# Kernel optimization log

Measured on AMD Instinct MI355X. Metric: run time of the kernel, lower is better.

Reference implementation:

```python
import jax, jax.numpy as jnp
import numpy as np

B, S, R, Z, NLHS = 1024, 277, 76, 56, 24  # batch, seq_len, n_rules, z_size, n_lhs_symbols


def setup_inputs() -> dict:
    key = jax.random.key(0)
    k1, k2, k3, k4, k5, k6 = jax.random.split(key, 6)
    model_out_x = jax.random.normal(k1, (B, S, R), jnp.float32)
    mu = jax.random.normal(k2, (B, Z), jnp.float32)
    log_var = 0.1 * jax.random.normal(k3, (B, Z), jnp.float32)
    # one-hot targets over rules
    tgt_idx = jax.random.randint(k4, (B, S), 0, R)
    target_x = jax.nn.one_hot(tgt_idx, R, dtype=jnp.float32)
    # binary allowed-transition masks per LHS symbol
    masks = (jax.random.uniform(k5, (NLHS, R)) < 0.3).astype(jnp.float32)
    masks = masks.at[:, 0].set(1.0)  # ensure no all-zero mask row
    ind_to_lhs_ind = jax.random.randint(k6, (R,), 0, NLHS)
    return dict(model_out_x=model_out_x, mu=mu, log_var=log_var,
                target_x=target_x, masks=masks, ind_to_lhs_ind=ind_to_lhs_ind)


def reference(model_out_x, mu, log_var, target_x, masks, ind_to_lhs_ind):
    b = model_out_x.shape[0]
    seq_len = model_out_x.shape[1]
    z_size = mu.shape[1]

    # --- apply_masks: vectorized gather replacing the nested python loops ---
    true_rule = jnp.argmax(target_x, axis=-1)          # [B,S]
    lhs = ind_to_lhs_ind[true_rule]                    # [B,S]
    mask = masks[lhs]                                  # [B,S,R]
    shift_to_tiny = -100.0 + (model_out_x.min() - model_out_x.max())
    x = model_out_x + (1.0 - mask) * shift_to_tiny

    # --- softmax + BCE (torch BCELoss clamps log terms at -100) ---
    p = jax.nn.softmax(x, axis=-1)
    log_p = jnp.maximum(jnp.log(p), -100.0)
    log_1mp = jnp.maximum(jnp.log1p(-p), -100.0)
    bce = -jnp.mean(target_x * log_p + (1.0 - target_x) * log_1mp)
    BCE = seq_len * bce

    # --- moment-matching error on mu ---
    avg_mu = jnp.sum(mu, axis=0) / b                   # [Z]
    var = (mu.T @ mu) / b                              # [Z,Z]
    var_err = var - jnp.eye(z_size, dtype=mu.dtype)
    var_err = jnp.tanh(var_err) * var_err
    mom_err = jnp.sum(avg_mu * avg_mu) / z_size + jnp.sum(var_err) / (z_size * z_size)

    # sample_z=False, module in training mode -> loss = BCE + mom_err
    return BCE + mom_err
```

## Files before the change

kernel.cpp:

```cpp
#include <hip/hip_runtime.h>
#include <math.h>

#define BB    1024
#define SS    277
#define RR    76
#define ZZ    56
#define NLHS  24
#define NROWS (BB*SS)
#define ROWS_PER_BLOCK 64
#define NBCE (NROWS/ROWS_PER_BLOCK)
#define NMOM ZZ
#define NBLK (NBCE + NMOM)
#define V4_PER_BLOCK (ROWS_PER_BLOCK*RR/4)
#define BLK_ELEMS (ROWS_PER_BLOCK*RR)
#define TOTAL_ELEMS 21558272.0

static_assert(NROWS % ROWS_PER_BLOCK == 0, "rows divide blocks");

#define LN2F  0.69314718056f
#define NLN2F (-144.26950409f)

__global__ __launch_bounds__(256) void fused_kernel(
    const float* __restrict__ model,
    const float* __restrict__ target,
    const float* __restrict__ masks,
    const int*   __restrict__ ind_to_lhs,
    const float* __restrict__ mu,
    double* __restrict__ partials)
{
    __shared__ float         sm_x[BLK_ELEMS];
    __shared__ unsigned int  smb[NLHS*4];
    __shared__ int           sm_lhs[RR];
    __shared__ unsigned char sm_idx[ROWS_PER_BLOCK];
    __shared__ float         sm_red[4];
    __shared__ float         sdot[4][64];
    __shared__ float         ssum[4];

    const int tid = threadIdx.x;

    if (blockIdx.x >= NBCE) {
        const int j    = blockIdx.x - NBCE;
        const int w    = tid >> 6;
        const int lane = tid & 63;
        const int i    = (lane < ZZ) ? lane : 0;
        float dot = 0.f, s1 = 0.f;
        const int b0 = 256*w;
        #pragma unroll 4
        for (int b = b0; b < b0 + 256; ++b) {
            const float c = mu[b*ZZ + j];
            const float a = mu[b*ZZ + i];
            dot = fmaf(a, c, dot);
            s1 += c;
        }
        sdot[w][lane] = dot;
        if (lane == 0) ssum[w] = s1;
        __syncthreads();
        if (w == 0) {
            float term = 0.f;
            if (lane < ZZ) {
                const float var = (sdot[0][lane]+sdot[1][lane]+sdot[2][lane]+sdot[3][lane]) * (1.f/BB);
                const float ve  = var - ((lane == j) ? 1.f : 0.f);
                term = tanhf(ve) * ve * (1.f/(ZZ*ZZ));
                if (lane == j) {
                    const float am = (ssum[0]+ssum[1]+ssum[2]+ssum[3]) * (1.f/BB);
                    term = fmaf(am*am, 1.f/ZZ, term);
                }
            }
            #pragma unroll
            for (int off = 32; off; off >>= 1) term += __shfl_xor(term, off, 64);
            if (lane == 0) partials[blockIdx.x] = (double)term;
        }
        return;
    }

    if (tid < NLHS*4) smb[tid] = 0u;
    if (tid < ROWS_PER_BLOCK) sm_idx[tid] = 0;
    __syncthreads();

    for (int e = tid; e < NLHS*RR; e += 256) {
        const int lhs = e / RR;
        const int r   = e - lhs*RR;
        if (masks[e] > 0.5f)
            atomicOr(&smb[lhs*4 + (r >> 5)], 1u << (r & 31));
    }
    if (tid < RR) sm_lhs[tid] = ind_to_lhs[tid];

    const size_t blk_base = (size_t)blockIdx.x * BLK_ELEMS;

    {
        const float4* m4  = (const float4*)(model + blk_base);
        float4*       sx4 = (float4*)sm_x;
        #pragma unroll
        for (int k = 0; k < 4; ++k) sx4[tid + 256*k] = m4[tid + 256*k];
        if (tid < V4_PER_BLOCK - 1024) sx4[1024 + tid] = m4[1024 + tid];
    }

    {
        const float4* t4 = (const float4*)(target + blk_base);
        #pragma unroll
        for (int k = 0; k < 5; ++k) {
            const int v4 = tid + 256*k;
            if (v4 < V4_PER_BLOCK) {
                const float4 t = t4[v4];
                int he = -1;
                const int e = v4*4;
                if (t.x > 0.5f) he = e;
                if (t.y > 0.5f) he = e+1;
                if (t.z > 0.5f) he = e+2;
                if (t.w > 0.5f) he = e+3;
                if (he >= 0) {
                    const int row = he / RR;
                    sm_idx[row] = (unsigned char)(he - row*RR);
                }
            }
        }
    }
    __syncthreads();

    const int row    = tid >> 2;
    const int t      = tid & 3;
    const int true_r = (int)sm_idx[row];
    const int lhs    = sm_lhs[true_r];
    const unsigned int w0 = smb[lhs*4 + 0];
    const unsigned int w1 = smb[lhs*4 + 1];
    const unsigned int w2 = smb[lhs*4 + 2];

    const float4* xr = (const float4*)(sm_x + row*RR);
    float4 v[5];

    float mx = -1e30f;
    #pragma unroll
    for (int k = 0; k < 5; ++k) {
        const int c = t + 4*k;
        float4 xv = (c < 19) ? xr[c] : make_float4(-1e30f,-1e30f,-1e30f,-1e30f);
        #pragma unroll
        for (int cc = 0; cc < 4; ++cc) {
            const int r = c*4 + cc;
            const unsigned int mw = (r < 32) ? w0 : ((r < 64) ? w1 : w2);
            float* xp = (&xv.x) + cc;
            const bool un = (r < RR) && ((mw >> (r & 31)) & 1u);
            const float xm = un ? *xp : -1e30f;
            *xp = xm;
            mx = fmaxf(mx, xm);
        }
        v[k] = xv;
    }
    mx = fmaxf(mx, __shfl_xor(mx, 1, 64));
    mx = fmaxf(mx, __shfl_xor(mx, 2, 64));

    float s = 0.f;
    #pragma unroll
    for (int k = 0; k < 5; ++k) {
        #pragma unroll
        for (int cc = 0; cc < 4; ++cc) {
            float* xp = (&v[k].x) + cc;
            const float e = __expf(*xp - mx);
            *xp = e;
            s += e;
        }
    }
    s += __shfl_xor(s, 1, 64);
    s += __shfl_xor(s, 2, 64);
    const float inv = 1.f / s;

    float sum_l2 = 0.f;
    float p_true = 0.f;
    bool  owner  = false;
    #pragma unroll
    for (int k = 0; k < 5; ++k) {
        const int c = t + 4*k;
        #pragma unroll
        for (int cc = 0; cc < 4; ++cc) {
            const int r = c*4 + cc;
            const float p  = (&v[k].x)[cc] * inv;
            const float l2 = __log2f(1.f - p);
            sum_l2 += fmaxf(l2, NLN2F);
            if (r == true_r) { p_true = p; owner = true; }
        }
    }
    float row_sum = LN2F * sum_l2;
    if (owner) {
        const float l1c_t = fmaxf(LN2F * __log2f(1.f - p_true), -100.f);
        const float lp_t  = fmaxf(__logf(p_true), -100.f);
        row_sum += lp_t - l1c_t;
    }

    #pragma unroll
    for (int off = 32; off; off >>= 1) row_sum += __shfl_xor(row_sum, off, 64);
    if ((tid & 63) == 0) sm_red[tid >> 6] = row_sum;
    __syncthreads();
    if (tid == 0)
        partials[blockIdx.x] = (double)((sm_red[0] + sm_red[1]) + (sm_red[2] + sm_red[3]));
}

__global__ __launch_bounds__(256) void final_kernel(
    const double* __restrict__ partials, float* __restrict__ out)
{
    __shared__ double sred[4];
    const int tid = threadIdx.x;
    double s = 0.0;
    for (int k = tid; k < NBCE; k += 256) s += partials[k];
    double m = (tid < NMOM) ? partials[NBCE + tid] : 0.0;
    double val = s * (-(double)SS / TOTAL_ELEMS) + m;
    #pragma unroll
    for (int off = 32; off; off >>= 1) val += __shfl_xor(val, off, 64);
    if ((tid & 63) == 0) sred[tid >> 6] = val;
    __syncthreads();
    if (tid == 0) out[0] = (float)((sred[0] + sred[1]) + (sred[2] + sred[3]));
}

extern "C" void kernel_launch(void* const* d_in, const int* in_sizes, int n_in,
                              void* d_out, int out_size, void* d_ws, size_t ws_size,
                              hipStream_t stream) {
    const float* model  = (const float*)d_in[0];
    const float* mu     = (const float*)d_in[1];
    const float* target = (const float*)d_in[3];
    const float* masks  = (const float*)d_in[4];
    const int*   ind    = (const int*)  d_in[5];
    float* out  = (float*)d_out;
    double* acc = (double*)d_ws;

    fused_kernel<<<NBLK, 256, 0, stream>>>(model, target, masks, ind, mu, acc);
    final_kernel<<<1,    256, 0, stream>>>(acc, out);
}
```

Baseline: 222.6 us.

## Load rows directly to registers and process four tiles per block with prefetch

Removes the shared-memory staging of model rows and the target scan into shared memory. Each thread now loads its row slice straight from global memory into registers and finds the true rule with a per-row shuffle reduction. Each block handles four 64-row tiles and prefetches the next tile into registers while computing the current one. This amortises the per-block mask-bitmap setup and lowers shared-memory use, but the per-thread global loads are strided by row and not coalesced, and register pressure goes up.

```diff
diff --git a/kernel.cpp b/kernel.cpp
--- a/kernel.cpp
+++ b/kernel.cpp
@@ -7,15 +7,15 @@
 #define ZZ    56
 #define NLHS  24
 #define NROWS (BB*SS)
-#define ROWS_PER_BLOCK 64
-#define NBCE (NROWS/ROWS_PER_BLOCK)
+#define ROWS_PER_TILE 64
+#define TT    4
+#define TILE_ELEMS (ROWS_PER_TILE*RR)
+#define NBCE (NROWS/(ROWS_PER_TILE*TT))
 #define NMOM ZZ
 #define NBLK (NBCE + NMOM)
-#define V4_PER_BLOCK (ROWS_PER_BLOCK*RR/4)
-#define BLK_ELEMS (ROWS_PER_BLOCK*RR)
 #define TOTAL_ELEMS 21558272.0
 
-static_assert(NROWS % ROWS_PER_BLOCK == 0, "rows divide blocks");
+static_assert(NROWS % (ROWS_PER_TILE*TT) == 0, "rows divide blocks");
 
 #define LN2F  0.69314718056f
 #define NLN2F (-144.26950409f)
@@ -28,13 +28,11 @@
     const float* __restrict__ mu,
     double* __restrict__ partials)
 {
-    __shared__ float         sm_x[BLK_ELEMS];
-    __shared__ unsigned int  smb[NLHS*4];
-    __shared__ int           sm_lhs[RR];
-    __shared__ unsigned char sm_idx[ROWS_PER_BLOCK];
-    __shared__ float         sm_red[4];
-    __shared__ float         sdot[4][64];
-    __shared__ float         ssum[4];
+    __shared__ uint4 smb[NLHS];
+    __shared__ int   sm_lhs[RR];
+    __shared__ float sm_red[4];
+    __shared__ float sdot[4][64];
+    __shared__ float ssum[4];
 
     const int tid = threadIdx.x;
 
@@ -73,121 +71,130 @@
         return;
     }
 
-    if (tid < NLHS*4) smb[tid] = 0u;
-    if (tid < ROWS_PER_BLOCK) sm_idx[tid] = 0;
-    __syncthreads();
-
+    if (tid < NLHS*4) ((unsigned int*)smb)[tid] = 0u;
+    __syncthreads();
     for (int e = tid; e < NLHS*RR; e += 256) {
         const int lhs = e / RR;
         const int r   = e - lhs*RR;
         if (masks[e] > 0.5f)
-            atomicOr(&smb[lhs*4 + (r >> 5)], 1u << (r & 31));
+            atomicOr(&((unsigned int*)smb)[lhs*4 + (r >> 5)], 1u << (r & 31));
     }
     if (tid < RR) sm_lhs[tid] = ind_to_lhs[tid];
-
-    const size_t blk_base = (size_t)blockIdx.x * BLK_ELEMS;
-
+    __syncthreads();
+
+    const int rloc = tid >> 2;
+    const int t    = tid & 3;
+
+    const size_t blk_elem0 = (size_t)blockIdx.x * (TT*TILE_ELEMS) + (size_t)rloc*RR;
+
+    float acc_thread = 0.f;
+
+    float4 v[5], tv[5];
     {
-        const float4* m4  = (const float4*)(model + blk_base);
-        float4*       sx4 = (float4*)sm_x;
-        #pragma unroll
-        for (int k = 0; k < 4; ++k) sx4[tid + 256*k] = m4[tid + 256*k];
-        if (tid < V4_PER_BLOCK - 1024) sx4[1024 + tid] = m4[1024 + tid];
-    }
-
-    {
-        const float4* t4 = (const float4*)(target + blk_base);
-        #pragma unroll
-        for (int k = 0; k < 5; ++k) {
-            const int v4 = tid + 256*k;
-            if (v4 < V4_PER_BLOCK) {
-                const float4 t = t4[v4];
-                int he = -1;
-                const int e = v4*4;
-                if (t.x > 0.5f) he = e;
-                if (t.y > 0.5f) he = e+1;
-                if (t.z > 0.5f) he = e+2;
-                if (t.w > 0.5f) he = e+3;
-                if (he >= 0) {
-                    const int row = he / RR;
-                    sm_idx[row] = (unsigned char)(he - row*RR);
-                }
-            }
-        }
-    }
-    __syncthreads();
-
-    const int row    = tid >> 2;
-    const int t      = tid & 3;
-    const int true_r = (int)sm_idx[row];
-    const int lhs    = sm_lhs[true_r];
-    const unsigned int w0 = smb[lhs*4 + 0];
-    const unsigned int w1 = smb[lhs*4 + 1];
-    const unsigned int w2 = smb[lhs*4 + 2];
-
-    const float4* xr = (const float4*)(sm_x + row*RR);
-    float4 v[5];
-
-    float mx = -1e30f;
+        const float4* mr = (const float4*)(model  + blk_elem0);
+        const float4* tr = (const float4*)(target + blk_elem0);
+        #pragma unroll
+        for (int k = 0; k < 5; ++k) {
+            const int c = t + 4*k;
+            v[k]  = (c < 19) ? mr[c] : make_float4(-1e30f,-1e30f,-1e30f,-1e30f);
+            tv[k] = (c < 19) ? tr[c] : make_float4(0.f,0.f,0.f,0.f);
+        }
+    }
+
     #pragma unroll
-    for (int k = 0; k < 5; ++k) {
-        const int c = t + 4*k;
-        float4 xv = (c < 19) ? xr[c] : make_float4(-1e30f,-1e30f,-1e30f,-1e30f);
-        #pragma unroll
-        for (int cc = 0; cc < 4; ++cc) {
-            const int r = c*4 + cc;
-            const unsigned int mw = (r < 32) ? w0 : ((r < 64) ? w1 : w2);
-            float* xp = (&xv.x) + cc;
-            const bool un = (r < RR) && ((mw >> (r & 31)) & 1u);
-            const float xm = un ? *xp : -1e30f;
-            *xp = xm;
-            mx = fmaxf(mx, xm);
-        }
-        v[k] = xv;
-    }
-    mx = fmaxf(mx, __shfl_xor(mx, 1, 64));
-    mx = fmaxf(mx, __shfl_xor(mx, 2, 64));
-
-    float s = 0.f;
+    for (int tt = 0; tt < TT; ++tt) {
+        float4 vn[5], tvn[5];
+        if (tt + 1 < TT) {
+            const size_t nb = blk_elem0 + (size_t)(tt+1)*TILE_ELEMS;
+            const float4* mr = (const float4*)(model  + nb);
+            const float4* tr = (const float4*)(target + nb);
+            #pragma unroll
+            for (int k = 0; k < 5; ++k) {
+                const int c = t + 4*k;
+                vn[k]  = (c < 19) ? mr[c] : make_float4(-1e30f,-1e30f,-1e30f,-1e30f);
+                tvn[k] = (c < 19) ? tr[c] : make_float4(0.f,0.f,0.f,0.f);
+            }
+        }
+
+        int he = -1;
+        #pragma unroll
+        for (int k = 0; k < 5; ++k) {
+            const int c = t + 4*k;
+            const int e = c*4;
+            if (tv[k].x > 0.5f) he = e;
+            if (tv[k].y > 0.5f) he = e+1;
+            if (tv[k].z > 0.5f) he = e+2;
+            if (tv[k].w > 0.5f) he = e+3;
+        }
+        he = max(he, __shfl_xor(he, 1, 64));
+        he = max(he, __shfl_xor(he, 2, 64));
+        const int true_r = he;
+
+        const int lhs = sm_lhs[true_r];
+        const uint4 mb = smb[lhs];
+        const unsigned int w0 = mb.x, w1 = mb.y, w2 = mb.z;
+
+        float mx = -1e30f;
+        #pragma unroll
+        for (int k = 0; k < 5; ++k) {
+            #pragma unroll
+            for (int cc = 0; cc < 4; ++cc) {
+                const int r = (t + 4*k)*4 + cc;
+                const unsigned int mw = (r < 32) ? w0 : ((r < 64) ? w1 : w2);
+                float* xp = (&v[k].x) + cc;
+                const bool un = (r < RR) && ((mw >> (r & 31)) & 1u);
+                const float xm = un ? *xp : -1e30f;
+                *xp = xm;
+                mx = fmaxf(mx, xm);
+            }
+        }
+        mx = fmaxf(mx, __shfl_xor(mx, 1, 64));
+        mx = fmaxf(mx, __shfl_xor(mx, 2, 64));
+
+        float s = 0.f;
+        #pragma unroll
+        for (int k = 0; k < 5; ++k) {
+            #pragma unroll
+            for (int cc = 0; cc < 4; ++cc) {
+                float* xp = (&v[k].x) + cc;
+                const float e = __expf(*xp - mx);
+                *xp = e;
+                s += e;
+            }
+        }
+        s += __shfl_xor(s, 1, 64);
+        s += __shfl_xor(s, 2, 64);
+        const float inv = 1.f / s;
+
+        float sum_l2 = 0.f;
+        float p_true = 0.f;
+        bool  owner  = false;
+        #pragma unroll
+        for (int k = 0; k < 5; ++k) {
+            #pragma unroll
+            for (int cc = 0; cc < 4; ++cc) {
+                const int r = (t + 4*k)*4 + cc;
+                const float p  = (&v[k].x)[cc] * inv;
+                const float l2 = __log2f(1.f - p);
+                sum_l2 += fmaxf(l2, NLN2F);
+                if (r == true_r) { p_true = p; owner = true; }
+            }
+        }
+        float part = LN2F * sum_l2;
+        if (owner) {
+            const float l1c_t = fmaxf(LN2F * __log2f(1.f - p_true), -100.f);
+            const float lp_t  = fmaxf(__logf(p_true), -100.f);
+            part += lp_t - l1c_t;
+        }
+        acc_thread += part;
+
+        #pragma unroll
+        for (int k = 0; k < 5; ++k) { v[k] = vn[k]; tv[k] = tvn[k]; }
+    }
+
     #pragma unroll
-    for (int k = 0; k < 5; ++k) {
-        #pragma unroll
-        for (int cc = 0; cc < 4; ++cc) {
-            float* xp = (&v[k].x) + cc;
-            const float e = __expf(*xp - mx);
-            *xp = e;
-            s += e;
-        }
-    }
-    s += __shfl_xor(s, 1, 64);
-    s += __shfl_xor(s, 2, 64);
-    const float inv = 1.f / s;
-
-    float sum_l2 = 0.f;
-    float p_true = 0.f;
-    bool  owner  = false;
-    #pragma unroll
-    for (int k = 0; k < 5; ++k) {
-        const int c = t + 4*k;
-        #pragma unroll
-        for (int cc = 0; cc < 4; ++cc) {
-            const int r = c*4 + cc;
-            const float p  = (&v[k].x)[cc] * inv;
-            const float l2 = __log2f(1.f - p);
-            sum_l2 += fmaxf(l2, NLN2F);
-            if (r == true_r) { p_true = p; owner = true; }
-        }
-    }
-    float row_sum = LN2F * sum_l2;
-    if (owner) {
-        const float l1c_t = fmaxf(LN2F * __log2f(1.f - p_true), -100.f);
-        const float lp_t  = fmaxf(__logf(p_true), -100.f);
-        row_sum += lp_t - l1c_t;
-    }
-
-    #pragma unroll
-    for (int off = 32; off; off >>= 1) row_sum += __shfl_xor(row_sum, off, 64);
-    if ((tid & 63) == 0) sm_red[tid >> 6] = row_sum;
+    for (int off = 32; off; off >>= 1) acc_thread += __shfl_xor(acc_thread, off, 64);
+    if ((tid & 63) == 0) sm_red[tid >> 6] = acc_thread;
     __syncthreads();
     if (tid == 0)
         partials[blockIdx.x] = (double)((sm_red[0] + sm_red[1]) + (sm_red[2] + sm_red[3]));
```

New measurement: 218.5 us. No clear change (-1.8%).
